# Performance work log

Measured on AMD Instinct MI355X. Metric: run time of the kernel, lower is better.

The kernel has to match this reference:

```python
import jax, jax.numpy as jnp
import numpy as np

N_TOKENS = 8192
D_MODEL = 2048
TOP_K = 2
N_S1 = N_TOKENS * TOP_K  # expanded (token, expert-slot) rows after top-k routing
N_S2 = 8192              # rows re-gathered for the second (intra-node) stage


def setup_inputs() -> dict:
    key = jax.random.key(0)
    k_x, k_i1, k_i2 = jax.random.split(key, 3)
    x = jax.random.normal(k_x, (N_TOKENS, D_MODEL), dtype=jnp.float32)
    # Expanded indices sorted by expert bin (upstream radix-sort of bin_ids).
    indices_s1 = jnp.sort(jax.random.randint(k_i1, (N_S1,), 0, N_S1, dtype=jnp.int64))
    # Map from s1-expert layout rows into the s2 stage layout.
    s1exp_to_s2_indices = jax.random.randint(k_i2, (N_S2,), 0, N_S1, dtype=jnp.int64)
    return {
        "x": x,
        "indices_s1": indices_s1,
        "s1exp_to_s2_indices": s1exp_to_s2_indices,
        "n_tokens": N_TOKENS,
        "top_k": TOP_K,
    }


def reference(x, indices_s1, s1exp_to_s2_indices, n_tokens, top_k):
    # Stage 1: gather_with_token_drop -- expanded index // top_k recovers the
    # source token row; rows are already ordered by expert bin (bins encode
    # capacity/drops, reflected in the length of indices_s1).
    dx_s1 = jnp.take(x, indices_s1 // top_k, axis=0)          # [N_S1, d]
    # _AllToAllSingle(ep_group): pure data exchange; on a single shard the
    # split-and-exchange with ins_s1/outs_s1 is the identity permutation.
    dx_s1_exp = dx_s1
    # Stage 2: s1_to_s2_gather -- re-gather rows into the intra-node layout
    # ordered by (bin_ids_s2, bins_s2).
    dx_s2 = jnp.take(dx_s1_exp, s1exp_to_s2_indices, axis=0)  # [N_S2, d]
    # _AllToAllSingle(local_group): identity on a single shard.
    dx_s2_exp = dx_s2
    # Final local ordering: s2 (intra-node) rows first, then s1 (global) rows.
    return jnp.concatenate([dx_s2_exp, dx_s1_exp], axis=0)    # [N_S2 + N_S1, d]
```

## Files before the change

kernel.cpp:

```cpp
#include <hip/hip_runtime.h>
#include <hip/hip_bf16.h>


typedef float v4f __attribute__((ext_vector_type(4)));

__global__ __launch_bounds__(256) void rb_dispatch_kernel(
    const float* __restrict__ x,
    const int* __restrict__ idx_s1,
    const int* __restrict__ idx_s2,
    const int* __restrict__ top_k_ptr,
    float* __restrict__ out,
    int n_s2, int n_rows, int nvec ) {
  const int wave = threadIdx.x >> 6;
  const int lane = threadIdx.x & 63;
  const int row = blockIdx.x * 4 + wave;
  if (row >= n_rows) return;

  const int top_k = *top_k_ptr;

  int src;
  if (row < n_s2) {
    src = idx_s1[idx_s2[row]] / top_k;
  } else {
    src = idx_s1[row - n_s2] / top_k;
  }

  const int d = nvec * 4;
  const v4f* __restrict__ sp = (const v4f*)(x + (size_t)src * (size_t)d);
  v4f* __restrict__ dp = (v4f*)(out + (size_t)row * (size_t)d);

  #pragma unroll 4
  for (int i = lane; i < nvec; i += 64) {
    v4f v = sp[i];
    __builtin_nontemporal_store(v, dp + i);
  }
}

extern "C" void kernel_launch(void* const* d_in, const int* in_sizes, int n_in,
                              void* d_out, int out_size, void* d_ws, size_t ws_size,
                              hipStream_t stream) {
  const float* x      = (const float*)d_in[0];
  const int*   idx_s1 = (const int*)d_in[1];
  const int*   idx_s2 = (const int*)d_in[2];
  const int*   top_k  = (const int*)d_in[4];
  float*       out    = (float*)d_out;

  const int n_s1   = in_sizes[1];
  const int n_s2   = in_sizes[2];
  const int n_rows = n_s1 + n_s2;
  const int d      = out_size / n_rows;
  const int nvec   = d / 4;

  const int rows_per_block = 4;
  const int grid = (n_rows + rows_per_block - 1) / rows_per_block;

  rb_dispatch_kernel<<<grid, 256, 0, stream>>>(
      x, idx_s1, idx_s2, top_k, out, n_s2, n_rows, nvec);
}
```

Measured before the change: 254.8 us.

## Split dispatch into specialized s1/s2 kernels with multi-row waves and full unroll

For d=2048 the single dispatch kernel is replaced by two kernels. The s1 kernel copies four rows per wave using a vectorized int4 index load. The s2 kernel copies two rows per wave. Each row copy is fully unrolled into eight 16-byte loads held in registers and issued before any store, which raises memory-level parallelism and removes the per-row branch. The cost is an extra kernel launch, fewer waves in flight per row, and the loss of generality, since other widths fall back to the generic kernel.

```diff
diff --git a/kernel.cpp b/kernel.cpp
--- a/kernel.cpp
+++ b/kernel.cpp
@@ -1,35 +1,88 @@
 #include <hip/hip_runtime.h>
-#include <hip/hip_bf16.h>
 
 
 typedef float v4f __attribute__((ext_vector_type(4)));
 
-__global__ __launch_bounds__(256) void rb_dispatch_kernel(
+__device__ __forceinline__ void copy_row_2048(const float* __restrict__ src,
+                                              float* __restrict__ dst,
+                                              int lane) {
+  const v4f* __restrict__ sp = (const v4f*)src;
+  v4f* __restrict__ dp = (v4f*)dst;
+  v4f t[8];
+#pragma unroll
+  for (int i = 0; i < 8; ++i) t[i] = sp[lane + 64 * i];
+#pragma unroll
+  for (int i = 0; i < 8; ++i)
+    __builtin_nontemporal_store(t[i], dp + lane + 64 * i);
+}
+
+__global__ __launch_bounds__(256) void rb_s1_kernel(
+    const float* __restrict__ x, const int* __restrict__ idx_s1,
+    const int* __restrict__ top_k_ptr, float* __restrict__ out_s1,
+    int n_s1) {
+  const int wave = threadIdx.x >> 6;
+  const int lane = threadIdx.x & 63;
+  const int r0 = (blockIdx.x * 4 + wave) * 4;
+  if (r0 >= n_s1) return;
+  const int tk = *top_k_ptr;
+
+  if (r0 + 3 < n_s1) {
+    const int4 iv = *(const int4*)(idx_s1 + r0);
+    int s[4] = {iv.x / tk, iv.y / tk, iv.z / tk, iv.w / tk};
+#pragma unroll
+    for (int k = 0; k < 4; ++k)
+      copy_row_2048(x + (size_t)s[k] * 2048,
+                    out_s1 + (size_t)(r0 + k) * 2048, lane);
+  } else {
+    for (int k = 0; k < 4 && r0 + k < n_s1; ++k) {
+      const int sv = idx_s1[r0 + k] / tk;
+      copy_row_2048(x + (size_t)sv * 2048,
+                    out_s1 + (size_t)(r0 + k) * 2048, lane);
+    }
+  }
+}
+
+__global__ __launch_bounds__(256) void rb_s2_kernel(
+    const float* __restrict__ x, const int* __restrict__ idx_s1,
+    const int* __restrict__ idx_s2, const int* __restrict__ top_k_ptr,
+    float* __restrict__ out, int n_s2) {
+  const int wave = threadIdx.x >> 6;
+  const int lane = threadIdx.x & 63;
+  const int r0 = (blockIdx.x * 4 + wave) * 2;
+  if (r0 >= n_s2) return;
+  const int tk = *top_k_ptr;
+
+  if (r0 + 1 < n_s2) {
+    const int2 jv = *(const int2*)(idx_s2 + r0);
+    const int s0 = idx_s1[jv.x] / tk;
+    const int s1 = idx_s1[jv.y] / tk;
+    copy_row_2048(x + (size_t)s0 * 2048, out + (size_t)r0 * 2048, lane);
+    copy_row_2048(x + (size_t)s1 * 2048, out + (size_t)(r0 + 1) * 2048, lane);
+  } else {
+    const int s0 = idx_s1[idx_s2[r0]] / tk;
+    copy_row_2048(x + (size_t)s0 * 2048, out + (size_t)r0 * 2048, lane);
+  }
+}
+
+__global__ __launch_bounds__(256) void rb_dispatch_generic(
     const float* __restrict__ x,
     const int* __restrict__ idx_s1,
     const int* __restrict__ idx_s2,
     const int* __restrict__ top_k_ptr,
     float* __restrict__ out,
-    int n_s2, int n_rows, int nvec ) {
+    int n_s2, int n_rows, int nvec) {
   const int wave = threadIdx.x >> 6;
   const int lane = threadIdx.x & 63;
   const int row = blockIdx.x * 4 + wave;
   if (row >= n_rows) return;
-
   const int top_k = *top_k_ptr;
-
   int src;
-  if (row < n_s2) {
-    src = idx_s1[idx_s2[row]] / top_k;
-  } else {
-    src = idx_s1[row - n_s2] / top_k;
-  }
-
+  if (row < n_s2) src = idx_s1[idx_s2[row]] / top_k;
+  else            src = idx_s1[row - n_s2] / top_k;
   const int d = nvec * 4;
   const v4f* __restrict__ sp = (const v4f*)(x + (size_t)src * (size_t)d);
   v4f* __restrict__ dp = (v4f*)(out + (size_t)row * (size_t)d);
-
-  #pragma unroll 4
+#pragma unroll 4
   for (int i = lane; i < nvec; i += 64) {
     v4f v = sp[i];
     __builtin_nontemporal_store(v, dp + i);
@@ -49,11 +102,18 @@
   const int n_s2   = in_sizes[2];
   const int n_rows = n_s1 + n_s2;
   const int d      = out_size / n_rows;
-  const int nvec   = d / 4;
 
-  const int rows_per_block = 4;
-  const int grid = (n_rows + rows_per_block - 1) / rows_per_block;
-
-  rb_dispatch_kernel<<<grid, 256, 0, stream>>>(
-      x, idx_s1, idx_s2, top_k, out, n_s2, n_rows, nvec);
+  if (d == 2048) {
+    const int grid1 = (n_s1 + 15) / 16;
+    rb_s1_kernel<<<grid1, 256, 0, stream>>>(
+        x, idx_s1, top_k, out + (size_t)n_s2 * 2048, n_s1);
+    const int grid2 = (n_s2 + 7) / 8;
+    rb_s2_kernel<<<grid2, 256, 0, stream>>>(
+        x, idx_s1, idx_s2, top_k, out, n_s2);
+  } else {
+    const int nvec = d / 4;
+    const int grid = (n_rows + 3) / 4;
+    rb_dispatch_generic<<<grid, 256, 0, stream>>>(
+        x, idx_s1, idx_s2, top_k, out, n_s2, n_rows, nvec);
+  }
 }
```

Result: no change. 258.6 us (+1.5%).

## Process four rows per wave with double-buffered register loads

Applied to the files above, without the earlier changes.

Adds a specialized kernel for d=2048 in which each wave copies four consecutive output rows. It resolves all four source indices first, then alternates two register buffers so the load of the next row is issued before the store of the previous one, and it fully unrolls with a compile-time row length. The goal is more memory-level parallelism and less per-row index-latency and loop overhead. The cost is higher register use, a grid four times smaller, and a generic fallback kept for other shapes.

```diff
diff --git a/kernel.cpp b/kernel.cpp
--- a/kernel.cpp
+++ b/kernel.cpp
@@ -1,35 +1,80 @@
 #include <hip/hip_runtime.h>
-#include <hip/hip_bf16.h>
 
 
 typedef float v4f __attribute__((ext_vector_type(4)));
 
-__global__ __launch_bounds__(256) void rb_dispatch_kernel(
+__device__ __forceinline__ void load_row(const float* __restrict__ src,
+                                         int lane, v4f t[8]) {
+  const v4f* __restrict__ sp = (const v4f*)src;
+#pragma unroll
+  for (int i = 0; i < 8; ++i) t[i] = sp[lane + 64 * i];
+}
+
+__device__ __forceinline__ void store_row_nt(float* __restrict__ dst,
+                                             int lane, const v4f t[8]) {
+  v4f* __restrict__ dp = (v4f*)dst;
+#pragma unroll
+  for (int i = 0; i < 8; ++i)
+    __builtin_nontemporal_store(t[i], dp + lane + 64 * i);
+}
+
+__global__ __launch_bounds__(256, 4) void rb_dispatch_r4(
     const float* __restrict__ x,
     const int* __restrict__ idx_s1,
     const int* __restrict__ idx_s2,
     const int* __restrict__ top_k_ptr,
     float* __restrict__ out,
-    int n_s2, int n_rows, int nvec ) {
+    int n_s2, int n_rows) {
+  const int wave = threadIdx.x >> 6;
+  const int lane = threadIdx.x & 63;
+  const int r0 = (blockIdx.x * 4 + wave) * 4;
+  if (r0 >= n_rows) return;
+  const int tk = *top_k_ptr;
+
+  int s[4];
+#pragma unroll
+  for (int k = 0; k < 4; ++k) {
+    const int r = r0 + k;
+    s[k] = (r < n_s2) ? (idx_s1[idx_s2[r]] / tk)
+                      : (idx_s1[r - n_s2] / tk);
+  }
+
+  const float* __restrict__ src0 = x + (size_t)s[0] * 2048;
+  const float* __restrict__ src1 = x + (size_t)s[1] * 2048;
+  const float* __restrict__ src2 = x + (size_t)s[2] * 2048;
+  const float* __restrict__ src3 = x + (size_t)s[3] * 2048;
+  float* __restrict__ dst = out + (size_t)r0 * 2048;
+
+  v4f A[8], B[8];
+  load_row(src0, lane, A);
+  load_row(src1, lane, B);
+  store_row_nt(dst + 0 * 2048, lane, A);
+  load_row(src2, lane, A);
+  store_row_nt(dst + 1 * 2048, lane, B);
+  load_row(src3, lane, B);
+  store_row_nt(dst + 2 * 2048, lane, A);
+  store_row_nt(dst + 3 * 2048, lane, B);
+}
+
+__global__ __launch_bounds__(256) void rb_dispatch_generic(
+    const float* __restrict__ x,
+    const int* __restrict__ idx_s1,
+    const int* __restrict__ idx_s2,
+    const int* __restrict__ top_k_ptr,
+    float* __restrict__ out,
+    int n_s2, int n_rows, int nvec) {
   const int wave = threadIdx.x >> 6;
   const int lane = threadIdx.x & 63;
   const int row = blockIdx.x * 4 + wave;
   if (row >= n_rows) return;
-
   const int top_k = *top_k_ptr;
-
   int src;
-  if (row < n_s2) {
-    src = idx_s1[idx_s2[row]] / top_k;
-  } else {
-    src = idx_s1[row - n_s2] / top_k;
-  }
-
+  if (row < n_s2) src = idx_s1[idx_s2[row]] / top_k;
+  else            src = idx_s1[row - n_s2] / top_k;
   const int d = nvec * 4;
   const v4f* __restrict__ sp = (const v4f*)(x + (size_t)src * (size_t)d);
   v4f* __restrict__ dp = (v4f*)(out + (size_t)row * (size_t)d);
-
-  #pragma unroll 4
+#pragma unroll 4
   for (int i = lane; i < nvec; i += 64) {
     v4f v = sp[i];
     __builtin_nontemporal_store(v, dp + i);
@@ -49,11 +94,15 @@
   const int n_s2   = in_sizes[2];
   const int n_rows = n_s1 + n_s2;
   const int d      = out_size / n_rows;
-  const int nvec   = d / 4;
 
-  const int rows_per_block = 4;
-  const int grid = (n_rows + rows_per_block - 1) / rows_per_block;
-
-  rb_dispatch_kernel<<<grid, 256, 0, stream>>>(
-      x, idx_s1, idx_s2, top_k, out, n_s2, n_rows, nvec);
+  if (d == 2048 && (n_rows & 3) == 0 && (n_s2 & 3) == 0) {
+    const int grid = n_rows / 16;
+    rb_dispatch_r4<<<grid, 256, 0, stream>>>(
+        x, idx_s1, idx_s2, top_k, out, n_s2, n_rows);
+  } else {
+    const int nvec = d / 4;
+    const int grid = (n_rows + 3) / 4;
+    rb_dispatch_generic<<<grid, 256, 0, stream>>>(
+        x, idx_s1, idx_s2, top_k, out, n_s2, n_rows, nvec);
+  }
 }
```

Result: no change. 255.2 us (+0.2%).
